# Kernel tuning notes

Hardware: AMD Instinct MI355X
Metric: run time of the kernel (lower is better)

## Reference

```python
import jax, jax.numpy as jnp
import numpy as np


def setup_inputs() -> dict:
    key = jax.random.key(0)
    k1, k2, k3 = jax.random.split(key, 3)
    B, S, D = 4, 2048, 4096
    C, E = 8, 8  # num_clusters, experts per cluster
    hidden_states = jax.random.normal(k1, (B, S, D), dtype=jnp.float32)
    W_cluster = jax.random.normal(k2, (C, D), dtype=jnp.float32) * 0.02
    W_experts = jax.random.normal(k3, (C, E, D), dtype=jnp.float32) * 0.02
    expert_ids = jnp.arange(C * E, dtype=jnp.int64).reshape(C, E)
    return {"hidden_states": hidden_states, "W_cluster": W_cluster,
            "W_experts": W_experts, "expert_ids": expert_ids}


def reference(hidden_states, W_cluster, W_experts, expert_ids):
    # hidden_states: [B, S, D]; W_cluster: [C, D]; W_experts: [C, E, D]; expert_ids: [C, E]
    B, S, D = hidden_states.shape
    C, E, _ = W_experts.shape
    num_total = C * E
    x = hidden_states.reshape(-1, D)                      # [T, D]
    T = x.shape[0]
    # First-level: token-level top-1 cluster routing (cluster_token_routing=True).
    # softmax is monotone, so argmax over logits == argmax over softmax weights.
    cluster_logits = x @ W_cluster.T                      # [T, C]
    cluster_idx = jnp.argmax(cluster_logits, axis=-1)     # [T]
    # Second-level: expert logits for every cluster, then gather the chosen cluster's.
    all_logits = jnp.einsum('td,ced->tce', x, W_experts)  # [T, C, E]
    rows = jnp.arange(T)
    sel_logits = all_logits[rows, cluster_idx]            # [T, E]
    cols = expert_ids[cluster_idx]                        # [T, E] global expert slots
    neg_min = jnp.finfo(hidden_states.dtype).min
    routing = jnp.full((T, num_total), neg_min, dtype=hidden_states.dtype)
    routing = routing.at[rows[:, None], cols].set(sel_logits)
    return routing.reshape(B, S, num_total)
```

## Files before the change

### kernel.cpp

```cpp
#include <hip/hip_runtime.h>
#include <cfloat>

#define DDIM 4096
#define NCLUS 8
#define NEXP 8
#define NOUT 64
#define NW 72
#define NCOL 80
#define FILL_BITS 0xFF7F0000u
#define WS_BYTES (8 * 16 * 5 * 64 * 16)

typedef float floatx4 __attribute__((ext_vector_type(4)));
typedef short bf16x8 __attribute__((ext_vector_type(8)));

__device__ __forceinline__ short bfh(float f) {
  return (short)(__float_as_uint(f) >> 16);
}
__device__ __forceinline__ bf16x8 pack8(const float4& a, const float4& b) {
  bf16x8 r;
  r[0] = bfh(a.x); r[1] = bfh(a.y); r[2] = bfh(a.z); r[3] = bfh(a.w);
  r[4] = bfh(b.x); r[5] = bfh(b.y); r[6] = bfh(b.z); r[7] = bfh(b.w);
  return r;
}

__global__ __launch_bounds__(256) void k_pack(const float* __restrict__ Wc,
                                              const float* __restrict__ We,
                                              bf16x8* __restrict__ ws) {
  const int gtid = blockIdx.x * 256 + threadIdx.x;
  const int frag = gtid >> 6;
  const int lane = gtid & 63;
  const int w = frag / 80;
  const int rem = frag % 80;
  const int s = rem / 5;
  const int ct = rem % 5;
  const int row = ct * 16 + (lane & 15);
  const int k = w * 512 + s * 32 + (lane >> 4) * 8;

  float4 b0 = {0.f, 0.f, 0.f, 0.f}, b1 = {0.f, 0.f, 0.f, 0.f};
  if (row < NW) {
    const float* rp = (row < NCLUS) ? (Wc + (size_t)row * DDIM)
                                    : (We + (size_t)(row - NCLUS) * DDIM);
    b0 = *(const float4*)(rp + k);
    b1 = *(const float4*)(rp + k + 4);
  }
  ws[gtid] = pack8(b0, b1);
}

template <bool USE_WS>
__global__ __launch_bounds__(512, 2) void k_mfma(const float* __restrict__ x,
                                                 const float* __restrict__ Wc,
                                                 const float* __restrict__ We,
                                                 const int* __restrict__ eids32,
                                                 const bf16x8* __restrict__ bws,
                                                 float* __restrict__ out) {
  __shared__ float s_acc[8][16 * NCOL];

  const int tid = threadIdx.x;
  const int lane = tid & 63;
  const int wave = tid >> 6;
  const int tile0 = blockIdx.x * 32;

  const int m = lane & 15;
  const int q = lane >> 4;
  const int kw = wave * 512 + q * 8;

  const float* xrow0 = x + (size_t)(tile0 + m) * DDIM + kw;
  const float* xrow1 = xrow0 + (size_t)16 * DDIM;
  const bf16x8* bbase = USE_WS ? (bws + (size_t)wave * 16 * 5 * 64 + lane) : nullptr;

  floatx4 acc0[5], acc1[5];
#pragma unroll
  for (int ct = 0; ct < 5; ++ct) {
    acc0[ct] = (floatx4){0.f, 0.f, 0.f, 0.f};
    acc1[ct] = (floatx4){0.f, 0.f, 0.f, 0.f};
  }

  if (USE_WS) {
    float4 pa[4][4];
    bf16x8 pb[3][5];

#pragma unroll
    for (int s = 0; s < 3; ++s) {
      const int kb = s * 32;
      pa[s][0] = *(const float4*)(xrow0 + kb);
      pa[s][1] = *(const float4*)(xrow0 + kb + 4);
      pa[s][2] = *(const float4*)(xrow1 + kb);
      pa[s][3] = *(const float4*)(xrow1 + kb + 4);
    }
#pragma unroll
    for (int s = 0; s < 2; ++s)
#pragma unroll
      for (int ct = 0; ct < 5; ++ct)
        pb[s][ct] = bbase[(s * 5 + ct) * 64];

#pragma unroll
    for (int step = 0; step < 16; ++step) {
      if (step + 3 < 16) {
        const int kb = (step + 3) * 32;
        const int sl = (step + 3) & 3;
        pa[sl][0] = *(const float4*)(xrow0 + kb);
        pa[sl][1] = *(const float4*)(xrow0 + kb + 4);
        pa[sl][2] = *(const float4*)(xrow1 + kb);
        pa[sl][3] = *(const float4*)(xrow1 + kb + 4);
      }
      if (step + 2 < 16) {
        const int sl = (step + 2) % 3;
#pragma unroll
        for (int ct = 0; ct < 5; ++ct)
          pb[sl][ct] = bbase[((step + 2) * 5 + ct) * 64];
      }

      const int sa = step & 3, sb = step % 3;
      const bf16x8 af0 = pack8(pa[sa][0], pa[sa][1]);
      const bf16x8 af1 = pack8(pa[sa][2], pa[sa][3]);
#pragma unroll
      for (int ct = 0; ct < 5; ++ct) {
        acc0[ct] = __builtin_amdgcn_mfma_f32_16x16x32_bf16(af0, pb[sb][ct], acc0[ct], 0, 0, 0);
        acc1[ct] = __builtin_amdgcn_mfma_f32_16x16x32_bf16(af1, pb[sb][ct], acc1[ct], 0, 0, 0);
      }
    }
  } else {
    float4 pa0 = *(const float4*)(xrow0);
    float4 pa1 = *(const float4*)(xrow0 + 4);
    float4 pc0 = *(const float4*)(xrow1);
    float4 pc1 = *(const float4*)(xrow1 + 4);
    float4 pb0[5], pb1[5];
#pragma unroll
    for (int ct = 0; ct < 5; ++ct) {
      const int wrow = ct * 16 + m;
      pb0[ct] = (float4){0.f, 0.f, 0.f, 0.f};
      pb1[ct] = (float4){0.f, 0.f, 0.f, 0.f};
      if (wrow < NW) {
        const float* bp = (wrow < NCLUS) ? (Wc + (size_t)wrow * DDIM)
                                         : (We + (size_t)(wrow - NCLUS) * DDIM);
        pb0[ct] = *(const float4*)(bp + kw);
        pb1[ct] = *(const float4*)(bp + kw + 4);
      }
    }
#pragma unroll
    for (int step = 0; step < 16; ++step) {
      const float4 ca0 = pa0, ca1 = pa1, cc0 = pc0, cc1 = pc1;
      bf16x8 cb[5];
#pragma unroll
      for (int ct = 0; ct < 5; ++ct) cb[ct] = pack8(pb0[ct], pb1[ct]);
      if (step < 15) {
        const int kb = (step + 1) * 32;
        pa0 = *(const float4*)(xrow0 + kb);
        pa1 = *(const float4*)(xrow0 + kb + 4);
        pc0 = *(const float4*)(xrow1 + kb);
        pc1 = *(const float4*)(xrow1 + kb + 4);
#pragma unroll
        for (int ct = 0; ct < 5; ++ct) {
          const int wrow = ct * 16 + m;
          if (wrow < NW) {
            const float* bp = (wrow < NCLUS) ? (Wc + (size_t)wrow * DDIM)
                                             : (We + (size_t)(wrow - NCLUS) * DDIM);
            pb0[ct] = *(const float4*)(bp + kw + kb);
            pb1[ct] = *(const float4*)(bp + kw + kb + 4);
          }
        }
      }
      const bf16x8 af0 = pack8(ca0, ca1);
      const bf16x8 af1 = pack8(cc0, cc1);
#pragma unroll
      for (int ct = 0; ct < 5; ++ct) {
        acc0[ct] = __builtin_amdgcn_mfma_f32_16x16x32_bf16(af0, cb[ct], acc0[ct], 0, 0, 0);
        acc1[ct] = __builtin_amdgcn_mfma_f32_16x16x32_bf16(af1, cb[ct], acc1[ct], 0, 0, 0);
      }
    }
  }

  const int is64 = (eids32[1] == 0) ? 1 : 0;
  const float fillv = __uint_as_float(FILL_BITS);

#pragma unroll
  for (int half = 0; half < 2; ++half) {
    if (half) __syncthreads();

#pragma unroll
    for (int ct = 0; ct < 5; ++ct)
#pragma unroll
      for (int r = 0; r < 4; ++r) {
        const floatx4& a = half ? acc1[ct] : acc0[ct];
        s_acc[wave][(q * 4 + r) * NCOL + ct * 16 + m] = a[r];
      }
    __syncthreads();

    for (int i = tid; i < 16 * NCOL; i += 512) {
      float s = s_acc[0][i];
#pragma unroll
      for (int w = 1; w < 8; ++w) s += s_acc[w][i];
      s_acc[0][i] = s;
    }
    __syncthreads();

    for (int idx = tid; idx < 16 * NOUT; idx += 512) {
      const int tok = idx >> 6;
      const int col = idx & 63;
      const float* P = &s_acc[0][tok * NCOL];
      float best = P[0];
      int c = 0;
#pragma unroll
      for (int cc = 1; cc < NCLUS; ++cc)
        if (P[cc] > best) { best = P[cc]; c = cc; }
      float val = fillv;
#pragma unroll
      for (int e = 0; e < NEXP; ++e) {
        const int slot = c * NEXP + e;
        const int ce = is64 ? eids32[slot << 1] : eids32[slot];
        if (ce == col) val = P[NCLUS + slot];
      }
      out[(size_t)(tile0 + half * 16 + tok) * NOUT + col] = val;
    }
  }
}

extern "C" void kernel_launch(void* const* d_in, const int* in_sizes, int n_in,
                              void* d_out, int out_size, void* d_ws, size_t ws_size,
                              hipStream_t stream) {
  const float* x = (const float*)d_in[0];
  const float* Wc = (const float*)d_in[1];
  const float* We = (const float*)d_in[2];
  const int* eids = (const int*)d_in[3];
  float* out = (float*)d_out;

  const int T = in_sizes[0] / DDIM;

  if (ws_size >= (size_t)WS_BYTES) {
    bf16x8* bws = (bf16x8*)d_ws;
    k_pack<<<160, 256, 0, stream>>>(Wc, We, bws);
    k_mfma<true><<<T / 32, 512, 0, stream>>>(x, Wc, We, eids, bws, out);
  } else {
    k_mfma<false><<<T / 32, 512, 0, stream>>>(x, Wc, We, eids, nullptr, out);
  }
}
```

Baseline: 204.8 us.

## Drop weight pre-pack kernel and load fp32 weights directly in MFMA loop

Removes the separate k_pack launch that converted the cluster and expert weights to bf16 fragments in the workspace. The GEMM kernel now reads fp32 weights straight from the inputs through a 2-deep prefetch buffer and converts them to bf16 in registers each step. Rows past 72 are clamped to a valid row instead of being zero-filled, and only the 64 expert columns are used downstream. This saves one kernel launch and the workspace round-trip, but every block now reads twice as many weight bytes and does extra per-step conversion work, which also raises register pressure.

```diff
diff --git a/kernel.cpp b/kernel.cpp
--- a/kernel.cpp
+++ b/kernel.cpp
@@ -8,7 +8,6 @@
 #define NW 72
 #define NCOL 80
 #define FILL_BITS 0xFF7F0000u
-#define WS_BYTES (8 * 16 * 5 * 64 * 16)
 
 typedef float floatx4 __attribute__((ext_vector_type(4)));
 typedef short bf16x8 __attribute__((ext_vector_type(8)));
@@ -23,35 +22,10 @@
   return r;
 }
 
-__global__ __launch_bounds__(256) void k_pack(const float* __restrict__ Wc,
-                                              const float* __restrict__ We,
-                                              bf16x8* __restrict__ ws) {
-  const int gtid = blockIdx.x * 256 + threadIdx.x;
-  const int frag = gtid >> 6;
-  const int lane = gtid & 63;
-  const int w = frag / 80;
-  const int rem = frag % 80;
-  const int s = rem / 5;
-  const int ct = rem % 5;
-  const int row = ct * 16 + (lane & 15);
-  const int k = w * 512 + s * 32 + (lane >> 4) * 8;
-
-  float4 b0 = {0.f, 0.f, 0.f, 0.f}, b1 = {0.f, 0.f, 0.f, 0.f};
-  if (row < NW) {
-    const float* rp = (row < NCLUS) ? (Wc + (size_t)row * DDIM)
-                                    : (We + (size_t)(row - NCLUS) * DDIM);
-    b0 = *(const float4*)(rp + k);
-    b1 = *(const float4*)(rp + k + 4);
-  }
-  ws[gtid] = pack8(b0, b1);
-}
-
-template <bool USE_WS>
 __global__ __launch_bounds__(512, 2) void k_mfma(const float* __restrict__ x,
                                                  const float* __restrict__ Wc,
                                                  const float* __restrict__ We,
                                                  const int* __restrict__ eids32,
-                                                 const bf16x8* __restrict__ bws,
                                                  float* __restrict__ out) {
   __shared__ float s_acc[8][16 * NCOL];
 
@@ -66,7 +40,15 @@
 
   const float* xrow0 = x + (size_t)(tile0 + m) * DDIM + kw;
   const float* xrow1 = xrow0 + (size_t)16 * DDIM;
-  const bf16x8* bbase = USE_WS ? (bws + (size_t)wave * 16 * 5 * 64 + lane) : nullptr;
+
+  const float* bp[5];
+#pragma unroll
+  for (int ct = 0; ct < 5; ++ct) {
+    int wrow = ct * 16 + m;
+    if (wrow >= NW) wrow = NW - 1;
+    bp[ct] = ((wrow < NCLUS) ? (Wc + (size_t)wrow * DDIM)
+                             : (We + (size_t)(wrow - NCLUS) * DDIM)) + kw;
+  }
 
   floatx4 acc0[5], acc1[5];
 #pragma unroll
@@ -75,98 +57,51 @@
     acc1[ct] = (floatx4){0.f, 0.f, 0.f, 0.f};
   }
 
-  if (USE_WS) {
-    float4 pa[4][4];
-    bf16x8 pb[3][5];
+  float4 pa[4][4];
+  float4 pbf[2][5][2];
 
 #pragma unroll
-    for (int s = 0; s < 3; ++s) {
-      const int kb = s * 32;
-      pa[s][0] = *(const float4*)(xrow0 + kb);
-      pa[s][1] = *(const float4*)(xrow0 + kb + 4);
-      pa[s][2] = *(const float4*)(xrow1 + kb);
-      pa[s][3] = *(const float4*)(xrow1 + kb + 4);
-    }
+  for (int s = 0; s < 3; ++s) {
+    const int kb = s * 32;
+    pa[s][0] = *(const float4*)(xrow0 + kb);
+    pa[s][1] = *(const float4*)(xrow0 + kb + 4);
+    pa[s][2] = *(const float4*)(xrow1 + kb);
+    pa[s][3] = *(const float4*)(xrow1 + kb + 4);
+  }
 #pragma unroll
-    for (int s = 0; s < 2; ++s)
-#pragma unroll
-      for (int ct = 0; ct < 5; ++ct)
-        pb[s][ct] = bbase[(s * 5 + ct) * 64];
+  for (int ct = 0; ct < 5; ++ct) {
+    pbf[0][ct][0] = *(const float4*)(bp[ct]);
+    pbf[0][ct][1] = *(const float4*)(bp[ct] + 4);
+  }
 
 #pragma unroll
-    for (int step = 0; step < 16; ++step) {
-      if (step + 3 < 16) {
-        const int kb = (step + 3) * 32;
-        const int sl = (step + 3) & 3;
-        pa[sl][0] = *(const float4*)(xrow0 + kb);
-        pa[sl][1] = *(const float4*)(xrow0 + kb + 4);
-        pa[sl][2] = *(const float4*)(xrow1 + kb);
-        pa[sl][3] = *(const float4*)(xrow1 + kb + 4);
-      }
-      if (step + 2 < 16) {
-        const int sl = (step + 2) % 3;
-#pragma unroll
-        for (int ct = 0; ct < 5; ++ct)
-          pb[sl][ct] = bbase[((step + 2) * 5 + ct) * 64];
-      }
-
-      const int sa = step & 3, sb = step % 3;
-      const bf16x8 af0 = pack8(pa[sa][0], pa[sa][1]);
-      const bf16x8 af1 = pack8(pa[sa][2], pa[sa][3]);
+  for (int step = 0; step < 16; ++step) {
+    if (step + 3 < 16) {
+      const int kb = (step + 3) * 32;
+      const int sl = (step + 3) & 3;
+      pa[sl][0] = *(const float4*)(xrow0 + kb);
+      pa[sl][1] = *(const float4*)(xrow0 + kb + 4);
+      pa[sl][2] = *(const float4*)(xrow1 + kb);
+      pa[sl][3] = *(const float4*)(xrow1 + kb + 4);
+    }
+    if (step + 1 < 16) {
+      const int kb = (step + 1) * 32;
+      const int sl = (step + 1) & 1;
 #pragma unroll
       for (int ct = 0; ct < 5; ++ct) {
-        acc0[ct] = __builtin_amdgcn_mfma_f32_16x16x32_bf16(af0, pb[sb][ct], acc0[ct], 0, 0, 0);
-        acc1[ct] = __builtin_amdgcn_mfma_f32_16x16x32_bf16(af1, pb[sb][ct], acc1[ct], 0, 0, 0);
+        pbf[sl][ct][0] = *(const float4*)(bp[ct] + kb);
+        pbf[sl][ct][1] = *(const float4*)(bp[ct] + kb + 4);
       }
     }
-  } else {
-    float4 pa0 = *(const float4*)(xrow0);
-    float4 pa1 = *(const float4*)(xrow0 + 4);
-    float4 pc0 = *(const float4*)(xrow1);
-    float4 pc1 = *(const float4*)(xrow1 + 4);
-    float4 pb0[5], pb1[5];
+
+    const int sa = step & 3, sb = step & 1;
+    const bf16x8 af0 = pack8(pa[sa][0], pa[sa][1]);
+    const bf16x8 af1 = pack8(pa[sa][2], pa[sa][3]);
 #pragma unroll
     for (int ct = 0; ct < 5; ++ct) {
-      const int wrow = ct * 16 + m;
-      pb0[ct] = (float4){0.f, 0.f, 0.f, 0.f};
-      pb1[ct] = (float4){0.f, 0.f, 0.f, 0.f};
-      if (wrow < NW) {
-        const float* bp = (wrow < NCLUS) ? (Wc + (size_t)wrow * DDIM)
-                                         : (We + (size_t)(wrow - NCLUS) * DDIM);
-        pb0[ct] = *(const float4*)(bp + kw);
-        pb1[ct] = *(const float4*)(bp + kw + 4);
-      }
-    }
-#pragma unroll
-    for (int step = 0; step < 16; ++step) {
-      const float4 ca0 = pa0, ca1 = pa1, cc0 = pc0, cc1 = pc1;
-      bf16x8 cb[5];
-#pragma unroll
-      for (int ct = 0; ct < 5; ++ct) cb[ct] = pack8(pb0[ct], pb1[ct]);
-      if (step < 15) {
-        const int kb = (step + 1) * 32;
-        pa0 = *(const float4*)(xrow0 + kb);
-        pa1 = *(const float4*)(xrow0 + kb + 4);
-        pc0 = *(const float4*)(xrow1 + kb);
-        pc1 = *(const float4*)(xrow1 + kb + 4);
-#pragma unroll
-        for (int ct = 0; ct < 5; ++ct) {
-          const int wrow = ct * 16 + m;
-          if (wrow < NW) {
-            const float* bp = (wrow < NCLUS) ? (Wc + (size_t)wrow * DDIM)
-                                             : (We + (size_t)(wrow - NCLUS) * DDIM);
-            pb0[ct] = *(const float4*)(bp + kw + kb);
-            pb1[ct] = *(const float4*)(bp + kw + kb + 4);
-          }
-        }
-      }
-      const bf16x8 af0 = pack8(ca0, ca1);
-      const bf16x8 af1 = pack8(cc0, cc1);
-#pragma unroll
-      for (int ct = 0; ct < 5; ++ct) {
-        acc0[ct] = __builtin_amdgcn_mfma_f32_16x16x32_bf16(af0, cb[ct], acc0[ct], 0, 0, 0);
-        acc1[ct] = __builtin_amdgcn_mfma_f32_16x16x32_bf16(af1, cb[ct], acc1[ct], 0, 0, 0);
-      }
+      const bf16x8 cb = pack8(pbf[sb][ct][0], pbf[sb][ct][1]);
+      acc0[ct] = __builtin_amdgcn_mfma_f32_16x16x32_bf16(af0, cb, acc0[ct], 0, 0, 0);
+      acc1[ct] = __builtin_amdgcn_mfma_f32_16x16x32_bf16(af1, cb, acc1[ct], 0, 0, 0);
     }
   }
 
@@ -225,12 +160,7 @@
   float* out = (float*)d_out;
 
   const int T = in_sizes[0] / DDIM;
+  (void)d_ws; (void)ws_size;
 
-  if (ws_size >= (size_t)WS_BYTES) {
-    bf16x8* bws = (bf16x8*)d_ws;
-    k_pack<<<160, 256, 0, stream>>>(Wc, We, bws);
-    k_mfma<true><<<T / 32, 512, 0, stream>>>(x, Wc, We, eids, bws, out);
-  } else {
-    k_mfma<false><<<T / 32, 512, 0, stream>>>(x, Wc, We, eids, nullptr, out);
-  }
+  k_mfma<<<T / 32, 512, 0, stream>>>(x, Wc, We, eids, out);
 }
```

New measurement: 227.3 us. +11.0%, slower.
